# Kernel optimization log

Hardware: AMD Instinct MI355X
Metric: run time of the kernel (lower is better)

## Reference

```python
import jax, jax.numpy as jnp
import numpy as np


def matmul_hadU(x):
    """Fast Walsh-Hadamard transform along the last dim (power of 2),
    normalized by 1/sqrt(n) — faithful translation of QuaRot's matmul_hadU
    radix-2 butterfly loop (Sylvester-ordered Hadamard)."""
    shape = x.shape
    n = shape[-1]
    assert (n & (n - 1)) == 0, "last dim must be a power of 2"
    b = x.reshape(-1, n, 1)  # (rows, m, t) with m*t == n throughout
    m, t = n, 1
    while m > 1:
        b = b.reshape(-1, m // 2, 2, t)
        lo = b[:, :, 0, :]
        hi = b[:, :, 1, :]
        b = jnp.stack([lo + hi, lo - hi], axis=2).reshape(-1, m // 2, 2 * t)
        m //= 2
        t *= 2
    scale = jnp.asarray(1.0 / np.sqrt(n), dtype=x.dtype)
    return b.reshape(shape) * scale


def setup_inputs() -> dict:
    key = jax.random.key(0)
    k1, k2, k3 = jax.random.split(key, 3)
    d = 2048
    x = jax.random.normal(k1, (4, 4096, d), dtype=jnp.float32)
    W = jax.random.normal(k2, (d, d), dtype=jnp.float32) * (1.0 / np.sqrt(d))
    b = jax.random.normal(k3, (d,), dtype=jnp.float32) * 0.01
    return {"x": x, "W": W, "b": b}


def reference(x, W, b):
    # R4Wrapper.forward: Hadamard-rotate x, then wrapped nn.Linear
    xr = matmul_hadU(x)                 # [B, S, D]
    return jnp.einsum("bsd,od->bso", xr, W) + b
```

## Files before the change

### kernel.cpp

```cpp
#include <hip/hip_runtime.h>
#include <stdint.h>

typedef __bf16 bf16x8 __attribute__((ext_vector_type(8)));
typedef float  f32x4  __attribute__((ext_vector_type(4)));
typedef unsigned short u16x8 __attribute__((ext_vector_type(8)));

__device__ __forceinline__ unsigned short f2bf(float f) {
    union { float f; unsigned int u; } v; v.f = f;
    unsigned int u = v.u;
    return (unsigned short)((u + 0x7FFFu + ((u >> 16) & 1u)) >> 16);
}

__global__ void cast_x_kernel(const float4* __restrict__ X,
                              u16x8* __restrict__ A, int n8) {
    int i = blockIdx.x * blockDim.x + threadIdx.x;
    if (i < n8) {
        float4 v0 = X[i * 2];
        float4 v1 = X[i * 2 + 1];
        u16x8 o;
        o[0] = f2bf(v0.x); o[1] = f2bf(v0.y); o[2] = f2bf(v0.z); o[3] = f2bf(v0.w);
        o[4] = f2bf(v1.x); o[5] = f2bf(v1.y); o[6] = f2bf(v1.z); o[7] = f2bf(v1.w);
        A[i] = o;
    }
}

__global__ void fwht_w_kernel(const float* __restrict__ W,
                              unsigned short* __restrict__ Bt) {
    const int n = 2048;
    __shared__ float buf[2048];
    const float* src = W + (size_t)blockIdx.x * n;
    for (int i = threadIdx.x; i < n; i += 256) buf[i] = src[i];
    __syncthreads();
    for (int len = 1; len < n; len <<= 1) {
        for (int j = threadIdx.x; j < n / 2; j += 256) {
            int idx = ((j & ~(len - 1)) << 1) | (j & (len - 1));
            float a = buf[idx], b = buf[idx + len];
            buf[idx]       = a + b;
            buf[idx + len] = a - b;
        }
        __syncthreads();
    }
    const float scale = 0.02209708691207961f;
    unsigned short* dst = Bt + (size_t)blockIdx.x * n;
    for (int i = threadIdx.x; i < n; i += 256) dst[i] = f2bf(buf[i] * scale);
}

__global__ __launch_bounds__(256) void had_gemm_kernel(
    const unsigned short* __restrict__ A,
    const unsigned short* __restrict__ B,
    const float* __restrict__ bias,
    float* __restrict__ C,
    int M, int N, int K)
{
    __shared__ __attribute__((aligned(16))) unsigned short As[2][128 * 32];
    __shared__ __attribute__((aligned(16))) unsigned short Bs[2][128 * 32];

    const int tid  = threadIdx.x;
    const int lane = tid & 63;
    const int wave = tid >> 6;
    const int m0 = blockIdx.y * 128;
    const int n0 = blockIdx.x * 128;
    const int wm = (wave & 1) * 64;
    const int wn = (wave >> 1) * 64;
    const int l16  = lane & 15;
    const int quad = lane >> 4;

    f32x4 acc[4][4] = {};

    const int c0 = wave * 2;
    const unsigned short* gA = A + (size_t)(m0 + c0 * 16 + (lane >> 2)) * K + (lane & 3) * 8;
    const unsigned short* gB = B + (size_t)(n0 + c0 * 16 + (lane >> 2)) * K + (lane & 3) * 8;
    const size_t rowStep = (size_t)16 * K;
    unsigned short* lA0 = &As[0][c0 * 512];
    unsigned short* lB0 = &Bs[0][c0 * 512];

    const unsigned short* pa = &As[0][(wm + l16) * 32 + quad * 8];
    const unsigned short* pb = &Bs[0][(wn + l16) * 32 + quad * 8];

    for (int k0 = 0; k0 < K; k0 += 64) {
        #pragma unroll
        for (int s = 0; s < 2; ++s) {
            #pragma unroll
            for (int c = 0; c < 2; ++c) {
                __builtin_amdgcn_global_load_lds(
                    (__attribute__((address_space(1))) const void*)(gA + k0 + s * 32 + c * rowStep),
                    (__attribute__((address_space(3))) void*)(lA0 + s * 4096 + c * 512), 16, 0, 0);
                __builtin_amdgcn_global_load_lds(
                    (__attribute__((address_space(1))) const void*)(gB + k0 + s * 32 + c * rowStep),
                    (__attribute__((address_space(3))) void*)(lB0 + s * 4096 + c * 512), 16, 0, 0);
            }
        }
        __syncthreads();

        #pragma unroll
        for (int s = 0; s < 2; ++s) {
            bf16x8 af[4], bfr[4];
            #pragma unroll
            for (int i = 0; i < 4; ++i) af[i]  = *(const bf16x8*)(pa + s * 4096 + i * 512);
            #pragma unroll
            for (int j = 0; j < 4; ++j) bfr[j] = *(const bf16x8*)(pb + s * 4096 + j * 512);
            #pragma unroll
            for (int i = 0; i < 4; ++i)
                #pragma unroll
                for (int j = 0; j < 4; ++j)
                    acc[i][j] = __builtin_amdgcn_mfma_f32_16x16x32_bf16(
                        af[i], bfr[j], acc[i][j], 0, 0, 0);
        }
        __syncthreads();
    }

    float bv[4];
    #pragma unroll
    for (int j = 0; j < 4; ++j) bv[j] = bias[n0 + wn + j * 16 + l16];

    #pragma unroll
    for (int i = 0; i < 4; ++i) {
        #pragma unroll
        for (int r = 0; r < 4; ++r) {
            int row = m0 + wm + i * 16 + quad * 4 + r;
            float* cp = C + (size_t)row * N + (n0 + wn + l16);
            #pragma unroll
            for (int j = 0; j < 4; ++j)
                cp[j * 16] = acc[i][j][r] + bv[j];
        }
    }
}

extern "C" void kernel_launch(void* const* d_in, const int* in_sizes, int n_in,
                              void* d_out, int out_size, void* d_ws, size_t ws_size,
                              hipStream_t stream) {
    const float* x = (const float*)d_in[0];
    const float* W = (const float*)d_in[1];
    const float* b = (const float*)d_in[2];
    float* out = (float*)d_out;

    const int d = in_sizes[2];
    const int M = in_sizes[0] / d;
    const int N = d, K = d;

    unsigned short* A_ws  = (unsigned short*)d_ws;
    unsigned short* Bt_ws = A_ws + (size_t)M * K;

    int n8 = in_sizes[0] / 8;
    cast_x_kernel<<<(n8 + 255) / 256, 256, 0, stream>>>(
        (const float4*)x, (u16x8*)A_ws, n8);

    fwht_w_kernel<<<N, 256, 0, stream>>>(W, Bt_ws);

    dim3 grid(N / 128, M / 128);
    had_gemm_kernel<<<grid, 256, 0, stream>>>(A_ws, Bt_ws, b, out, M, N, K);
}
```

Baseline: 388.2 us.

## Use 256x256 GEMM tiles with 4-stage LDS pipeline and swizzled layout

Replaces the 128x128 single-buffered GEMM with a 256x256 tile processed by 8 waves. The new loop keeps a 4-deep ring of async global-to-LDS loads with explicit vmcnt waits, XOR-swizzles the LDS layout to cut bank conflicts, and splits each K step into two half-phases, raising priority around the MFMA blocks. The aim is to hide global load latency and raise data reuse per block. In exchange it uses 128KB of LDS and more accumulator registers, which limits occupancy, and it hardcodes K=N=2048.

```diff
diff --git a/kernel.cpp b/kernel.cpp
--- a/kernel.cpp
+++ b/kernel.cpp
@@ -45,80 +45,127 @@
     for (int i = threadIdx.x; i < n; i += 256) dst[i] = f2bf(buf[i] * scale);
 }
 
-__global__ __launch_bounds__(256) void had_gemm_kernel(
+constexpr int GK = 2048;
+constexpr int GN = 2048;
+constexpr int NT = GK / 32;
+
+__global__ __launch_bounds__(512, 2) void had_gemm_kernel(
     const unsigned short* __restrict__ A,
     const unsigned short* __restrict__ B,
     const float* __restrict__ bias,
-    float* __restrict__ C,
-    int M, int N, int K)
+    float* __restrict__ C)
 {
-    __shared__ __attribute__((aligned(16))) unsigned short As[2][128 * 32];
-    __shared__ __attribute__((aligned(16))) unsigned short Bs[2][128 * 32];
+    __shared__ __attribute__((aligned(16))) unsigned short As[4][256 * 32];
+    __shared__ __attribute__((aligned(16))) unsigned short Bs[4][256 * 32];
 
     const int tid  = threadIdx.x;
     const int lane = tid & 63;
     const int wave = tid >> 6;
-    const int m0 = blockIdx.y * 128;
-    const int n0 = blockIdx.x * 128;
-    const int wm = (wave & 1) * 64;
-    const int wn = (wave >> 1) * 64;
+    const int wm   = wave & 1;
+    const int wn   = wave >> 1;
     const int l16  = lane & 15;
     const int quad = lane >> 4;
+    const int m0 = blockIdx.y * 256;
+    const int n0 = blockIdx.x * 256;
 
-    f32x4 acc[4][4] = {};
+    f32x4 acc[8][4] = {};
 
-    const int c0 = wave * 2;
-    const unsigned short* gA = A + (size_t)(m0 + c0 * 16 + (lane >> 2)) * K + (lane & 3) * 8;
-    const unsigned short* gB = B + (size_t)(n0 + c0 * 16 + (lane >> 2)) * K + (lane & 3) * 8;
-    const size_t rowStep = (size_t)16 * K;
-    unsigned short* lA0 = &As[0][c0 * 512];
-    unsigned short* lB0 = &Bs[0][c0 * 512];
+    const int srow = tid >> 2;
+    const int swzc = ((tid & 3) * 16) ^ (((srow >> 1) & 3) << 4);
+    const char* gA0 = (const char*)(A + (size_t)(m0 + srow) * GK) + swzc;
+    const char* gA1 = (const char*)(A + (size_t)(m0 + 128 + srow) * GK) + swzc;
+    const char* gB0 = (const char*)(B + (size_t)(n0 + srow) * GK) + swzc;
+    const char* gB1 = (const char*)(B + (size_t)(n0 + 128 + srow) * GK) + swzc;
 
-    const unsigned short* pa = &As[0][(wm + l16) * 32 + quad * 8];
-    const unsigned short* pb = &Bs[0][(wn + l16) * 32 + quad * 8];
+#define STAGE_A(t_) { const int sl_ = (t_) & 3;                                   \
+    __builtin_amdgcn_global_load_lds(                                             \
+        (const __attribute__((address_space(1))) void*)(gA0 + (t_) * 64),         \
+        (__attribute__((address_space(3))) void*)(&As[sl_][wave * 512]), 16, 0, 0);\
+    __builtin_amdgcn_global_load_lds(                                             \
+        (const __attribute__((address_space(1))) void*)(gA1 + (t_) * 64),         \
+        (__attribute__((address_space(3))) void*)(&As[sl_][4096 + wave * 512]), 16, 0, 0); }
+#define STAGE_B(t_) { const int sl_ = (t_) & 3;                                   \
+    __builtin_amdgcn_global_load_lds(                                             \
+        (const __attribute__((address_space(1))) void*)(gB0 + (t_) * 64),         \
+        (__attribute__((address_space(3))) void*)(&Bs[sl_][wave * 512]), 16, 0, 0);\
+    __builtin_amdgcn_global_load_lds(                                             \
+        (const __attribute__((address_space(1))) void*)(gB1 + (t_) * 64),         \
+        (__attribute__((address_space(3))) void*)(&Bs[sl_][4096 + wave * 512]), 16, 0, 0); }
 
-    for (int k0 = 0; k0 < K; k0 += 64) {
+    const int arow = wm * 128 + l16;
+    const int brow = wn * 64 + l16;
+    const int sw   = ((l16 >> 1) & 3) << 4;
+    const unsigned aoff = (unsigned)(arow * 64 + quad * 16) ^ sw;
+    const unsigned boff = (unsigned)(brow * 64 + quad * 16) ^ sw;
+    const char* sabase = (const char*)&As[0][0];
+    const char* sbbase = (const char*)&Bs[0][0];
+
+    STAGE_A(0) STAGE_B(0) asm volatile("" ::: "memory");
+    STAGE_A(1) STAGE_B(1) asm volatile("" ::: "memory");
+    STAGE_A(2) STAGE_B(2)
+    asm volatile("s_waitcnt vmcnt(8)" ::: "memory");
+    __builtin_amdgcn_s_barrier();
+    asm volatile("" ::: "memory");
+
+    for (int t = 0; t < NT; ++t) {
+        const char* sa = sabase + (size_t)(t & 3) * 16384;
+        const char* sb = sbbase + (size_t)(t & 3) * 16384;
+        bf16x8 af[4], bfr[4];
+
+        if (t + 3 < NT) STAGE_A(t + 3);
         #pragma unroll
-        for (int s = 0; s < 2; ++s) {
+        for (int j = 0; j < 4; ++j)
+            bfr[j] = *(const bf16x8*)(sb + (boff + j * 1024u));
+        #pragma unroll
+        for (int i = 0; i < 4; ++i)
+            af[i] = *(const bf16x8*)(sa + (aoff + i * 1024u));
+        asm volatile("" ::: "memory");
+        __builtin_amdgcn_s_barrier();
+        __builtin_amdgcn_s_setprio(1);
+        #pragma unroll
+        for (int i = 0; i < 4; ++i)
             #pragma unroll
-            for (int c = 0; c < 2; ++c) {
-                __builtin_amdgcn_global_load_lds(
-                    (__attribute__((address_space(1))) const void*)(gA + k0 + s * 32 + c * rowStep),
-                    (__attribute__((address_space(3))) void*)(lA0 + s * 4096 + c * 512), 16, 0, 0);
-                __builtin_amdgcn_global_load_lds(
-                    (__attribute__((address_space(1))) const void*)(gB + k0 + s * 32 + c * rowStep),
-                    (__attribute__((address_space(3))) void*)(lB0 + s * 4096 + c * 512), 16, 0, 0);
-            }
-        }
-        __syncthreads();
+            for (int j = 0; j < 4; ++j)
+                acc[i][j] = __builtin_amdgcn_mfma_f32_16x16x32_bf16(
+                    af[i], bfr[j], acc[i][j], 0, 0, 0);
+        __builtin_amdgcn_s_setprio(0);
+        __builtin_amdgcn_s_barrier();
+        asm volatile("" ::: "memory");
 
+        if (t + 3 < NT) STAGE_B(t + 3);
         #pragma unroll
-        for (int s = 0; s < 2; ++s) {
-            bf16x8 af[4], bfr[4];
+        for (int i = 0; i < 4; ++i)
+            af[i] = *(const bf16x8*)(sa + (aoff + (4 + i) * 1024u));
+        asm volatile("" ::: "memory");
+        __builtin_amdgcn_s_barrier();
+        __builtin_amdgcn_s_setprio(1);
+        #pragma unroll
+        for (int i = 0; i < 4; ++i)
             #pragma unroll
-            for (int i = 0; i < 4; ++i) af[i]  = *(const bf16x8*)(pa + s * 4096 + i * 512);
-            #pragma unroll
-            for (int j = 0; j < 4; ++j) bfr[j] = *(const bf16x8*)(pb + s * 4096 + j * 512);
-            #pragma unroll
-            for (int i = 0; i < 4; ++i)
-                #pragma unroll
-                for (int j = 0; j < 4; ++j)
-                    acc[i][j] = __builtin_amdgcn_mfma_f32_16x16x32_bf16(
-                        af[i], bfr[j], acc[i][j], 0, 0, 0);
-        }
-        __syncthreads();
+            for (int j = 0; j < 4; ++j)
+                acc[4 + i][j] = __builtin_amdgcn_mfma_f32_16x16x32_bf16(
+                    af[i], bfr[j], acc[4 + i][j], 0, 0, 0);
+        __builtin_amdgcn_s_setprio(0);
+
+        if (t < NT - 3)       { asm volatile("s_waitcnt vmcnt(8)" ::: "memory"); }
+        else if (t == NT - 3) { asm volatile("s_waitcnt vmcnt(4)" ::: "memory"); }
+        else if (t == NT - 2) { asm volatile("s_waitcnt vmcnt(0)" ::: "memory"); }
+        __builtin_amdgcn_s_barrier();
+        asm volatile("" ::: "memory");
     }
+#undef STAGE_A
+#undef STAGE_B
 
     float bv[4];
     #pragma unroll
-    for (int j = 0; j < 4; ++j) bv[j] = bias[n0 + wn + j * 16 + l16];
+    for (int j = 0; j < 4; ++j) bv[j] = bias[n0 + wn * 64 + j * 16 + l16];
 
     #pragma unroll
-    for (int i = 0; i < 4; ++i) {
+    for (int i = 0; i < 8; ++i) {
         #pragma unroll
         for (int r = 0; r < 4; ++r) {
-            int row = m0 + wm + i * 16 + quad * 4 + r;
-            float* cp = C + (size_t)row * N + (n0 + wn + l16);
+            int row = m0 + wm * 128 + i * 16 + quad * 4 + r;
+            float* cp = C + (size_t)row * GN + (n0 + wn * 64 + l16);
             #pragma unroll
             for (int j = 0; j < 4; ++j)
                 cp[j * 16] = acc[i][j][r] + bv[j];
@@ -147,6 +194,6 @@
 
     fwht_w_kernel<<<N, 256, 0, stream>>>(W, Bt_ws);
 
-    dim3 grid(N / 128, M / 128);
-    had_gemm_kernel<<<grid, 256, 0, stream>>>(A_ws, Bt_ws, b, out, M, N, K);
+    dim3 grid(N / 256, M / 256);
+    had_gemm_kernel<<<grid, 512, 0, stream>>>(A_ws, Bt_ws, b, out);
 }
```

Result: slower. 406.2 us (+4.7%).
